# Performance work log

Hardware: AMD Instinct MI355X
Metric: run time of the kernel (lower is better)

## Reference

```python
import jax, jax.numpy as jnp
import numpy as np

N = 50000   # nodes
E = 600000  # edges (avg degree 12)
D = 128     # node feature dim (input == hidden so residual applies)
R = 7       # num_relation
G = 32      # num graphs in the batch
L = 3       # layers
W_SCALE = 0.02


def setup_inputs() -> dict:
    key = jax.random.key(0)
    ks = jax.random.split(key, 5 + 2 * L)
    inp = {
        "x": jax.random.normal(ks[0], (N, D), jnp.float32),
        "node_in": jax.random.randint(ks[1], (E,), 0, N),
        "node_out": jax.random.randint(ks[2], (E,), 0, N),
        "relation": jax.random.randint(ks[3], (E,), 0, R),
        "edge_weight": jnp.ones((E,), jnp.float32),
        "node2graph": jnp.sort(jax.random.randint(ks[4], (N,), 0, G)),
        "num_node": N,
        "num_graphs": G,
    }
    for i in range(L):
        inp[f"sl_w{i}"] = jax.random.normal(ks[5 + 2 * i], (D, D), jnp.float32) * W_SCALE
        inp[f"sl_b{i}"] = jnp.zeros((D,), jnp.float32)
        inp[f"lin_w{i}"] = jax.random.normal(ks[6 + 2 * i], (R * D, D), jnp.float32) * W_SCALE
        inp[f"lin_b{i}"] = jnp.zeros((D,), jnp.float32)
    return inp


def _gearnet(x, edge_weight, params, node_in, node_out, relation, node2graph,
             num_node, num_graphs):
    # relation-keyed scatter index: node_out * R + relation
    idx = node_out * R + relation  # [E]
    h = x
    for (sl_w, sl_b, lin_w, lin_b) in params:
        din = h.shape[1]
        msg = h[node_in] * edge_weight[:, None]                           # [E, din] gather
        agg = jax.ops.segment_sum(msg, idx, num_segments=num_node * R)    # [N*R, din] scatter_add
        upd = agg.reshape(num_node, R * din)                              # [N, R*din]
        out = jax.nn.relu(upd @ lin_w + lin_b + h @ sl_w + sl_b)          # combine: linear + self_loop, relu
        h = out + h                                                        # short_cut residual (shapes match)
    node_feature = h
    graph_feature = jax.ops.segment_sum(node_feature, node2graph, num_segments=num_graphs)  # SumReadout
    return graph_feature, node_feature


def reference(x, node_in, node_out, relation, edge_weight, node2graph,
              sl_w0, sl_b0, lin_w0, lin_b0,
              sl_w1, sl_b1, lin_w1, lin_b1,
              sl_w2, sl_b2, lin_w2, lin_b2,
              num_node, num_graphs):
    params = [(sl_w0, sl_b0, lin_w0, lin_b0),
              (sl_w1, sl_b1, lin_w1, lin_b1),
              (sl_w2, sl_b2, lin_w2, lin_b2)]
    return _gearnet(x, edge_weight, params, node_in, node_out, relation,
                    node2graph, num_node, num_graphs)
```

## Files before the change

### kernel.cpp

```cpp
#include <hip/hip_runtime.h>
#include <hip/hip_bf16.h>

#define NN 50000
#define EE 600000
#define DD 128
#define RR 7
#define SS 8
#define GG 32
#define NSEG (NN * RR)
#define NB1 ((NSEG + 1023) / 1024)

typedef float f32x4 __attribute__((ext_vector_type(4)));
typedef float f32x2 __attribute__((ext_vector_type(2)));
typedef short short8 __attribute__((ext_vector_type(8)));
typedef unsigned short u16x8 __attribute__((ext_vector_type(8)));

static __device__ __forceinline__ unsigned short f2bf(float f) {
    union { float f; unsigned u; } v; v.f = f;
    unsigned r = v.u + 0x7fff + ((v.u >> 16) & 1);
    return (unsigned short)(r >> 16);
}
static __device__ __forceinline__ float bf2f(unsigned short u) {
    union { unsigned u; float f; } v; v.u = ((unsigned)u) << 16;
    return v.f;
}

__global__ void prep_w2(const float* __restrict__ lin_w, const float* __restrict__ sl_w,
                        const float* __restrict__ lin_b, const float* __restrict__ sl_b,
                        unsigned short* __restrict__ Wt2, float* __restrict__ bias) {
    int idx = blockIdx.x * 256 + threadIdx.x;
    if (idx < DD) bias[idx] = lin_b[idx] + sl_b[idx];
    if (idx >= 1024 * DD) return;
    int j = idx >> 7;
    int k = idx & 127;
    int slot = j >> 7, dout = j & 127;
    float w = (slot < 7) ? lin_w[(slot * DD + k) * DD + dout] : sl_w[k * DD + dout];
    Wt2[(size_t)j * DD + k] = f2bf(w);
}

__global__ void zero_misc(int* __restrict__ cc, int* __restrict__ slop, float* __restrict__ gf) {
    int i = blockIdx.x * 256 + threadIdx.x;
    if (i < 2 * NSEG) cc[i] = 0;
    if (i < 16) slop[i] = 0;
    if (i < GG * DD) gf[i] = 0.f;
}

__global__ void hist(const int* __restrict__ node_out, const int* __restrict__ rel,
                     int* __restrict__ counts) {
    int e = blockIdx.x * 256 + threadIdx.x;
    if (e >= EE) return;
    atomicAdd(&counts[node_out[e] * RR + rel[e]], 1);
}

__global__ __launch_bounds__(256) void scan1(const int* __restrict__ counts,
                                             int* __restrict__ start, int* __restrict__ bsum) {
    __shared__ int s[256];
    int tid = threadIdx.x;
    int base = blockIdx.x * 1024 + tid * 4;
    int v[4], sum = 0;
    #pragma unroll
    for (int j = 0; j < 4; ++j) {
        v[j] = (base + j < NSEG) ? counts[base + j] : 0;
        sum += v[j];
    }
    s[tid] = sum; __syncthreads();
    for (int off = 1; off < 256; off <<= 1) {
        int t = (tid >= off) ? s[tid - off] : 0;
        __syncthreads();
        s[tid] += t;
        __syncthreads();
    }
    int run = s[tid] - sum;
    if (tid == 255) bsum[blockIdx.x] = s[255];
    #pragma unroll
    for (int j = 0; j < 4; ++j) {
        if (base + j < NSEG) { start[base + j] = run; run += v[j]; }
    }
}

__global__ __launch_bounds__(512) void scan2(int* __restrict__ bsum) {
    __shared__ int s[512];
    int tid = threadIdx.x;
    int v = (tid < NB1) ? bsum[tid] : 0;
    s[tid] = v; __syncthreads();
    for (int off = 1; off < 512; off <<= 1) {
        int t = (tid >= off) ? s[tid - off] : 0;
        __syncthreads();
        s[tid] += t;
        __syncthreads();
    }
    if (tid < NB1) bsum[tid] = s[tid] - v;
}

__global__ void scan3(const int* __restrict__ start, const int* __restrict__ bsum,
                      const int* __restrict__ counts, int2* __restrict__ segd) {
    int i = blockIdx.x * 256 + threadIdx.x;
    if (i < NSEG) segd[i] = make_int2(start[i] + bsum[i >> 10], counts[i]);
}

__global__ void fill(const int* __restrict__ node_in, const int* __restrict__ node_out,
                     const int* __restrict__ rel, const float* __restrict__ ew,
                     const int2* __restrict__ segd, int* __restrict__ cursor,
                     int2* __restrict__ edges) {
    int e = blockIdx.x * 256 + threadIdx.x;
    if (e >= EE) return;
    int seg = node_out[e] * RR + rel[e];
    int pos = segd[seg].x + atomicAdd(&cursor[seg], 1);
    edges[pos] = make_int2((rel[e] << 16) | node_in[e], __float_as_int(ew[e]));
}

__global__ void init_hb(const float* __restrict__ x, unsigned short* __restrict__ hb) {
    int t = blockIdx.x * 256 + threadIdx.x;
    if (t >= NN * 32) return;
    f32x4 v = ((const f32x4*)x)[t];
    unsigned long long pack = (unsigned long long)f2bf(v.x)
                            | ((unsigned long long)f2bf(v.y) << 16)
                            | ((unsigned long long)f2bf(v.z) << 32)
                            | ((unsigned long long)f2bf(v.w) << 48);
    ((unsigned long long*)hb)[t] = pack;
}

__global__ __launch_bounds__(256) void gemm_p(
        const unsigned short* __restrict__ hb,
        const unsigned short* __restrict__ Wt2,
        unsigned short* __restrict__ P) {
    int tid = threadIdx.x;
    int wid = tid >> 6, lane = tid & 63;
    int wr = wid >> 1, wc = wid & 1;
    int lm = lane & 15, lg = lane >> 4;
    int bm0 = blockIdx.x * 128;

    short8 af[4][4];
    #pragma unroll
    for (int mi = 0; mi < 4; ++mi) {
        int gr = bm0 + wr * 64 + mi * 16 + lm;
        #pragma unroll
        for (int ks = 0; ks < 4; ++ks) {
            short8 t = {};
            if (gr < NN) t = *(const short8*)(hb + (size_t)gr * DD + ks * 32 + lg * 8);
            af[mi][ks] = t;
        }
    }
    for (int cb = 0; cb < 8; ++cb) {
        f32x4 acc[4][4] = {};
        #pragma unroll
        for (int ks = 0; ks < 4; ++ks) {
            short8 bfr[4];
            #pragma unroll
            for (int ni = 0; ni < 4; ++ni)
                bfr[ni] = *(const short8*)(Wt2 + (size_t)(cb * 128 + wc * 64 + ni * 16 + lm) * DD
                                           + ks * 32 + lg * 8);
            #pragma unroll
            for (int mi = 0; mi < 4; ++mi)
                #pragma unroll
                for (int ni = 0; ni < 4; ++ni)
                    acc[mi][ni] = __builtin_amdgcn_mfma_f32_16x16x32_bf16(af[mi][ks], bfr[ni], acc[mi][ni], 0, 0, 0);
        }
        #pragma unroll
        for (int mi = 0; mi < 4; ++mi) {
            #pragma unroll
            for (int v = 0; v < 4; ++v) {
                int gm = bm0 + wr * 64 + mi * 16 + lg * 4 + v;
                if (gm >= NN) continue;
                #pragma unroll
                for (int ni = 0; ni < 4; ++ni) {
                    int j = cb * 128 + wc * 64 + ni * 16 + lm;
                    P[(size_t)gm * 1024 + j] = f2bf(acc[mi][ni][v]);
                }
            }
        }
    }
}

#define PROW(r) (const unsigned*)(P + (size_t)((((r).x & 0xFFFF) << 3) | ((r).x >> 16)) * DD + lane * 2)
__global__ __launch_bounds__(256) void gather_p(
        const unsigned short* __restrict__ P,
        const int2* __restrict__ segd,
        const int2* __restrict__ edges,
        const float* __restrict__ bias,
        const unsigned short* __restrict__ hb_in,
        unsigned short* __restrict__ hb_out,
        float* __restrict__ nf,
        int last) {
    int tid = threadIdx.x;
    int wv = tid >> 6, lane = tid & 63;
    int node = blockIdx.x * 4 + wv;
    int st = segd[node * RR].x;
    int2 s6 = segd[node * RR + 6];
    int end = s6.x + s6.y;

    float ax = 0.f, ay = 0.f;
    int2 r0 = edges[st];
    int2 r1 = edges[st + 1];
    int2 r2 = edges[st + 2];
    int2 r3 = edges[st + 3];
    int2 r4 = edges[st + 4];
    unsigned hv0 = *PROW(r0);
    unsigned hv1 = *PROW(r1);
    unsigned hv2 = *PROW(r2);
    unsigned hv3 = *PROW(r3);
    for (int i = st; i < end; ++i) {
        int2 r5 = edges[i + 5];
        unsigned hv4 = *PROW(r4);
        float w = __int_as_float(r0.y);
        ax += bf2f((unsigned short)(hv0 & 0xFFFF)) * w;
        ay += bf2f((unsigned short)(hv0 >> 16)) * w;
        r0 = r1; r1 = r2; r2 = r3; r3 = r4; r4 = r5;
        hv0 = hv1; hv1 = hv2; hv2 = hv3; hv3 = hv4;
    }
    unsigned hs = *(const unsigned*)(P + ((size_t)node * 8 + 7) * DD + lane * 2);
    float bx = bias[lane * 2], by = bias[lane * 2 + 1];
    unsigned hp = ((const unsigned*)hb_in)[(size_t)node * 64 + lane];
    float hpx = bf2f((unsigned short)(hp & 0xFFFF));
    float hpy = bf2f((unsigned short)(hp >> 16));
    float vx = fmaxf(ax + bf2f((unsigned short)(hs & 0xFFFF)) + bx, 0.f) + hpx;
    float vy = fmaxf(ay + bf2f((unsigned short)(hs >> 16)) + by, 0.f) + hpy;
    if (last)
        ((f32x2*)nf)[(size_t)node * 64 + lane] = (f32x2){vx, vy};
    else
        ((unsigned*)hb_out)[(size_t)node * 64 + lane] =
            (unsigned)f2bf(vx) | ((unsigned)f2bf(vy) << 16);
}

__global__ __launch_bounds__(256) void readout(const float* __restrict__ h,
                                               const int* __restrict__ n2g,
                                               float* __restrict__ gf) {
    int c0 = blockIdx.x * 128;
    int rg = threadIdx.x >> 5, d4 = threadIdx.x & 31;
    f32x4 acc = {0.f, 0.f, 0.f, 0.f};
    int cur = -1;
    #pragma unroll 4
    for (int it = 0; it < 16; ++it) {
        int row = c0 + it * 8 + rg;
        if (row >= NN) break;
        int g = n2g[row];
        if (g != cur) {
            if (cur >= 0) {
                atomicAdd(&gf[cur * DD + d4 * 4 + 0], acc.x);
                atomicAdd(&gf[cur * DD + d4 * 4 + 1], acc.y);
                atomicAdd(&gf[cur * DD + d4 * 4 + 2], acc.z);
                atomicAdd(&gf[cur * DD + d4 * 4 + 3], acc.w);
            }
            cur = g;
            acc = (f32x4){0.f, 0.f, 0.f, 0.f};
        }
        acc += ((const f32x4*)h)[(size_t)row * 32 + d4];
    }
    if (cur >= 0) {
        atomicAdd(&gf[cur * DD + d4 * 4 + 0], acc.x);
        atomicAdd(&gf[cur * DD + d4 * 4 + 1], acc.y);
        atomicAdd(&gf[cur * DD + d4 * 4 + 2], acc.z);
        atomicAdd(&gf[cur * DD + d4 * 4 + 3], acc.w);
    }
}

extern "C" void kernel_launch(void* const* d_in, const int* in_sizes, int n_in,
                              void* d_out, int out_size, void* d_ws, size_t ws_size,
                              hipStream_t stream) {
    const float* x      = (const float*)d_in[0];
    const int* node_in  = (const int*)d_in[1];
    const int* node_out = (const int*)d_in[2];
    const int* relation = (const int*)d_in[3];
    const float* ew     = (const float*)d_in[4];
    const int* n2g      = (const int*)d_in[5];
    const float* sl_w[3]  = {(const float*)d_in[8],  (const float*)d_in[12], (const float*)d_in[16]};
    const float* sl_b[3]  = {(const float*)d_in[9],  (const float*)d_in[13], (const float*)d_in[17]};
    const float* lin_w[3] = {(const float*)d_in[10], (const float*)d_in[14], (const float*)d_in[18]};
    const float* lin_b[3] = {(const float*)d_in[11], (const float*)d_in[15], (const float*)d_in[19]};

    float* out = (float*)d_out;
    float* gf = out;
    float* nf = out + GG * DD;

    char* ws = (char*)d_ws;
    size_t off = 0;
    unsigned short* P  = (unsigned short*)(ws + off); off += (size_t)NN * 1024 * 2;
    unsigned short* hb0 = (unsigned short*)(ws + off); off += (size_t)NN * DD * 2;
    unsigned short* hb1 = (unsigned short*)(ws + off); off += (size_t)NN * DD * 2;
    unsigned short* Wt2 = (unsigned short*)(ws + off); off += (size_t)3 * 1024 * DD * 2;
    float* bias = (float*)(ws + off);            off += 3 * DD * 4;
    int* counts = (int*)(ws + off);              off += (size_t)NSEG * 4;
    int* cursor = (int*)(ws + off);              off += (size_t)NSEG * 4;
    int* start  = (int*)(ws + off);              off += (size_t)NSEG * 4;
    int2* segd  = (int2*)(ws + off);             off += (size_t)NSEG * 8;
    int* bsum   = (int*)(ws + off);              off += 512 * 4;
    int2* edges = (int2*)(ws + off);             off += (size_t)(EE + 8) * 8;

    for (int l = 0; l < 3; ++l)
        prep_w2<<<512, 256, 0, stream>>>(lin_w[l], sl_w[l], lin_b[l], sl_b[l],
                                         Wt2 + (size_t)l * 1024 * DD, bias + l * DD);

    zero_misc<<<(2 * NSEG + 255) / 256, 256, 0, stream>>>(counts, (int*)(edges + EE), gf);
    hist<<<(EE + 255) / 256, 256, 0, stream>>>(node_out, relation, counts);
    scan1<<<NB1, 256, 0, stream>>>(counts, start, bsum);
    scan2<<<1, 512, 0, stream>>>(bsum);
    scan3<<<(NSEG + 255) / 256, 256, 0, stream>>>(start, bsum, counts, segd);
    fill<<<(EE + 255) / 256, 256, 0, stream>>>(node_in, node_out, relation, ew,
                                               segd, cursor, edges);
    init_hb<<<(NN * 32) / 256, 256, 0, stream>>>(x, hb0);

    unsigned short* hbs[2] = { hb0, hb1 };
    for (int l = 0; l < 3; ++l) {
        gemm_p<<<(NN + 127) / 128, 256, 0, stream>>>(
            hbs[l & 1], Wt2 + (size_t)l * 1024 * DD, P);
        gather_p<<<NN / 4, 256, 0, stream>>>(
            P, segd, edges, bias + l * DD, hbs[l & 1], hbs[(l + 1) & 1],
            nf, l == 2 ? 1 : 0);
    }
    readout<<<(NN + 127) / 128, 256, 0, stream>>>(nf, n2g, gf);
}
```

Baseline: 392.7 us.

## Bucket edges per destination node and split gather across half-waves

Edge CSR is now keyed by destination node instead of node*relation, which shrinks the histogram, scan and segment arrays sevenfold. The gather kernel has each half-wave process alternate edges with 8-byte loads of four features per lane, then combines the halves with a cross-lane shuffle. The three weight-prep launches are merged into one. Summation order within a node changes and the half-wave split adds predication for odd edge counts.

After: 364.3 us (median of 2 runs). 1.08x faster.

```diff
diff --git a/kernel.cpp b/kernel.cpp
--- a/kernel.cpp
+++ b/kernel.cpp
@@ -5,15 +5,12 @@
 #define EE 600000
 #define DD 128
 #define RR 7
-#define SS 8
 #define GG 32
-#define NSEG (NN * RR)
-#define NB1 ((NSEG + 1023) / 1024)
+#define NB1 ((NN + 1023) / 1024)
 
 typedef float f32x4 __attribute__((ext_vector_type(4)));
 typedef float f32x2 __attribute__((ext_vector_type(2)));
 typedef short short8 __attribute__((ext_vector_type(8)));
-typedef unsigned short u16x8 __attribute__((ext_vector_type(8)));
 
 static __device__ __forceinline__ unsigned short f2bf(float f) {
     union { float f; unsigned u; } v; v.f = f;
@@ -25,31 +22,39 @@
     return v.f;
 }
 
-__global__ void prep_w2(const float* __restrict__ lin_w, const float* __restrict__ sl_w,
-                        const float* __restrict__ lin_b, const float* __restrict__ sl_b,
+__global__ void prep_w2(const float* lw0, const float* lw1, const float* lw2,
+                        const float* sw0, const float* sw1, const float* sw2,
+                        const float* lb0, const float* lb1, const float* lb2,
+                        const float* sb0, const float* sb1, const float* sb2,
                         unsigned short* __restrict__ Wt2, float* __restrict__ bias) {
-    int idx = blockIdx.x * 256 + threadIdx.x;
-    if (idx < DD) bias[idx] = lin_b[idx] + sl_b[idx];
+    int l = blockIdx.x >> 9;
+    int idx = (blockIdx.x & 511) * 256 + threadIdx.x;
+    const float* lin_w = l == 0 ? lw0 : (l == 1 ? lw1 : lw2);
+    const float* sl_w  = l == 0 ? sw0 : (l == 1 ? sw1 : sw2);
+    if (idx < DD) {
+        const float* lin_b = l == 0 ? lb0 : (l == 1 ? lb1 : lb2);
+        const float* sl_b  = l == 0 ? sb0 : (l == 1 ? sb1 : sb2);
+        bias[l * DD + idx] = lin_b[idx] + sl_b[idx];
+    }
     if (idx >= 1024 * DD) return;
     int j = idx >> 7;
     int k = idx & 127;
     int slot = j >> 7, dout = j & 127;
     float w = (slot < 7) ? lin_w[(slot * DD + k) * DD + dout] : sl_w[k * DD + dout];
-    Wt2[(size_t)j * DD + k] = f2bf(w);
+    Wt2[(size_t)l * 1024 * DD + (size_t)j * DD + k] = f2bf(w);
 }
 
 __global__ void zero_misc(int* __restrict__ cc, int* __restrict__ slop, float* __restrict__ gf) {
     int i = blockIdx.x * 256 + threadIdx.x;
-    if (i < 2 * NSEG) cc[i] = 0;
+    if (i < 2 * NN) cc[i] = 0;
     if (i < 16) slop[i] = 0;
     if (i < GG * DD) gf[i] = 0.f;
 }
 
-__global__ void hist(const int* __restrict__ node_out, const int* __restrict__ rel,
-                     int* __restrict__ counts) {
+__global__ void hist(const int* __restrict__ node_out, int* __restrict__ counts) {
     int e = blockIdx.x * 256 + threadIdx.x;
     if (e >= EE) return;
-    atomicAdd(&counts[node_out[e] * RR + rel[e]], 1);
+    atomicAdd(&counts[node_out[e]], 1);
 }
 
 __global__ __launch_bounds__(256) void scan1(const int* __restrict__ counts,
@@ -60,7 +65,7 @@
     int v[4], sum = 0;
     #pragma unroll
     for (int j = 0; j < 4; ++j) {
-        v[j] = (base + j < NSEG) ? counts[base + j] : 0;
+        v[j] = (base + j < NN) ? counts[base + j] : 0;
         sum += v[j];
     }
     s[tid] = sum; __syncthreads();
@@ -74,16 +79,16 @@
     if (tid == 255) bsum[blockIdx.x] = s[255];
     #pragma unroll
     for (int j = 0; j < 4; ++j) {
-        if (base + j < NSEG) { start[base + j] = run; run += v[j]; }
-    }
-}
-
-__global__ __launch_bounds__(512) void scan2(int* __restrict__ bsum) {
-    __shared__ int s[512];
+        if (base + j < NN) { start[base + j] = run; run += v[j]; }
+    }
+}
+
+__global__ __launch_bounds__(64) void scan2(int* __restrict__ bsum) {
+    __shared__ int s[64];
     int tid = threadIdx.x;
     int v = (tid < NB1) ? bsum[tid] : 0;
     s[tid] = v; __syncthreads();
-    for (int off = 1; off < 512; off <<= 1) {
+    for (int off = 1; off < 64; off <<= 1) {
         int t = (tid >= off) ? s[tid - off] : 0;
         __syncthreads();
         s[tid] += t;
@@ -95,7 +100,7 @@
 __global__ void scan3(const int* __restrict__ start, const int* __restrict__ bsum,
                       const int* __restrict__ counts, int2* __restrict__ segd) {
     int i = blockIdx.x * 256 + threadIdx.x;
-    if (i < NSEG) segd[i] = make_int2(start[i] + bsum[i >> 10], counts[i]);
+    if (i < NN) segd[i] = make_int2(start[i] + bsum[i >> 10], counts[i]);
 }
 
 __global__ void fill(const int* __restrict__ node_in, const int* __restrict__ node_out,
@@ -104,7 +109,7 @@
                      int2* __restrict__ edges) {
     int e = blockIdx.x * 256 + threadIdx.x;
     if (e >= EE) return;
-    int seg = node_out[e] * RR + rel[e];
+    int seg = node_out[e];
     int pos = segd[seg].x + atomicAdd(&cursor[seg], 1);
     edges[pos] = make_int2((rel[e] << 16) | node_in[e], __float_as_int(ew[e]));
 }
@@ -172,7 +177,7 @@
     }
 }
 
-#define PROW(r) (const unsigned*)(P + (size_t)((((r).x & 0xFFFF) << 3) | ((r).x >> 16)) * DD + lane * 2)
+#define PR(r) ((const uint2*)(P + (size_t)(((((r).x & 0xFFFF) << 3) | ((r).x >> 16))) * DD) + l5)
 __global__ __launch_bounds__(256) void gather_p(
         const unsigned short* __restrict__ P,
         const int2* __restrict__ segd,
@@ -184,42 +189,54 @@
         int last) {
     int tid = threadIdx.x;
     int wv = tid >> 6, lane = tid & 63;
+    int h = lane >> 5, l5 = lane & 31;
     int node = blockIdx.x * 4 + wv;
-    int st = segd[node * RR].x;
-    int2 s6 = segd[node * RR + 6];
-    int end = s6.x + s6.y;
-
-    float ax = 0.f, ay = 0.f;
-    int2 r0 = edges[st];
-    int2 r1 = edges[st + 1];
-    int2 r2 = edges[st + 2];
-    int2 r3 = edges[st + 3];
-    int2 r4 = edges[st + 4];
-    unsigned hv0 = *PROW(r0);
-    unsigned hv1 = *PROW(r1);
-    unsigned hv2 = *PROW(r2);
-    unsigned hv3 = *PROW(r3);
-    for (int i = st; i < end; ++i) {
-        int2 r5 = edges[i + 5];
-        unsigned hv4 = *PROW(r4);
-        float w = __int_as_float(r0.y);
-        ax += bf2f((unsigned short)(hv0 & 0xFFFF)) * w;
-        ay += bf2f((unsigned short)(hv0 >> 16)) * w;
-        r0 = r1; r1 = r2; r2 = r3; r3 = r4; r4 = r5;
-        hv0 = hv1; hv1 = hv2; hv2 = hv3; hv3 = hv4;
-    }
-    unsigned hs = *(const unsigned*)(P + ((size_t)node * 8 + 7) * DD + lane * 2);
-    float bx = bias[lane * 2], by = bias[lane * 2 + 1];
-    unsigned hp = ((const unsigned*)hb_in)[(size_t)node * 64 + lane];
-    float hpx = bf2f((unsigned short)(hp & 0xFFFF));
-    float hpy = bf2f((unsigned short)(hp >> 16));
-    float vx = fmaxf(ax + bf2f((unsigned short)(hs & 0xFFFF)) + bx, 0.f) + hpx;
-    float vy = fmaxf(ay + bf2f((unsigned short)(hs >> 16)) + by, 0.f) + hpy;
-    if (last)
-        ((f32x2*)nf)[(size_t)node * 64 + lane] = (f32x2){vx, vy};
-    else
-        ((unsigned*)hb_out)[(size_t)node * 64 + lane] =
-            (unsigned)f2bf(vx) | ((unsigned)f2bf(vy) << 16);
+    int2 sd = segd[node];
+    int st = sd.x, cnt = sd.y;
+    int base = st + h;
+    int mmax = (cnt + 1) >> 1;
+
+    f32x4 ac = {0.f, 0.f, 0.f, 0.f};
+    int2 r0 = edges[base];
+    int2 r1 = edges[base + 2];
+    int2 r2 = edges[base + 4];
+    uint2 hv0 = *PR(r0);
+    uint2 hv1 = *PR(r1);
+    for (int i = 0; i < mmax; ++i) {
+        int2 r3 = edges[base + 2 * i + 6];
+        uint2 hv2 = *PR(r2);
+        if (h + 2 * i < cnt) {
+            float w = __int_as_float(r0.y);
+            ac.x += bf2f((unsigned short)(hv0.x & 0xFFFF)) * w;
+            ac.y += bf2f((unsigned short)(hv0.x >> 16)) * w;
+            ac.z += bf2f((unsigned short)(hv0.y & 0xFFFF)) * w;
+            ac.w += bf2f((unsigned short)(hv0.y >> 16)) * w;
+        }
+        r0 = r1; r1 = r2; r2 = r3;
+        hv0 = hv1; hv1 = hv2;
+    }
+    ac.x += __shfl_xor(ac.x, 32);
+    ac.y += __shfl_xor(ac.y, 32);
+    ac.z += __shfl_xor(ac.z, 32);
+    ac.w += __shfl_xor(ac.w, 32);
+
+    if (h == 0) {
+        uint2 hs = *((const uint2*)(P + ((size_t)node * 8 + 7) * DD) + l5);
+        f32x4 b4 = ((const f32x4*)bias)[l5];
+        uint2 hp = ((const uint2*)hb_in)[(size_t)node * 32 + l5];
+        float o0 = fmaxf(ac.x + bf2f((unsigned short)(hs.x & 0xFFFF)) + b4.x, 0.f) + bf2f((unsigned short)(hp.x & 0xFFFF));
+        float o1 = fmaxf(ac.y + bf2f((unsigned short)(hs.x >> 16))   + b4.y, 0.f) + bf2f((unsigned short)(hp.x >> 16));
+        float o2 = fmaxf(ac.z + bf2f((unsigned short)(hs.y & 0xFFFF)) + b4.z, 0.f) + bf2f((unsigned short)(hp.y & 0xFFFF));
+        float o3 = fmaxf(ac.w + bf2f((unsigned short)(hs.y >> 16))   + b4.w, 0.f) + bf2f((unsigned short)(hp.y >> 16));
+        if (last) {
+            ((f32x4*)nf)[(size_t)node * 32 + l5] = (f32x4){o0, o1, o2, o3};
+        } else {
+            uint2 pk;
+            pk.x = (unsigned)f2bf(o0) | ((unsigned)f2bf(o1) << 16);
+            pk.y = (unsigned)f2bf(o2) | ((unsigned)f2bf(o3) << 16);
+            ((uint2*)hb_out)[(size_t)node * 32 + l5] = pk;
+        }
+    }
 }
 
 __global__ __launch_bounds__(256) void readout(const float* __restrict__ h,
@@ -263,10 +280,6 @@
     const int* relation = (const int*)d_in[3];
     const float* ew     = (const float*)d_in[4];
     const int* n2g      = (const int*)d_in[5];
-    const float* sl_w[3]  = {(const float*)d_in[8],  (const float*)d_in[12], (const float*)d_in[16]};
-    const float* sl_b[3]  = {(const float*)d_in[9],  (const float*)d_in[13], (const float*)d_in[17]};
-    const float* lin_w[3] = {(const float*)d_in[10], (const float*)d_in[14], (const float*)d_in[18]};
-    const float* lin_b[3] = {(const float*)d_in[11], (const float*)d_in[15], (const float*)d_in[19]};
 
     float* out = (float*)d_out;
     float* gf = out;
@@ -279,22 +292,25 @@
     unsigned short* hb1 = (unsigned short*)(ws + off); off += (size_t)NN * DD * 2;
     unsigned short* Wt2 = (unsigned short*)(ws + off); off += (size_t)3 * 1024 * DD * 2;
     float* bias = (float*)(ws + off);            off += 3 * DD * 4;
-    int* counts = (int*)(ws + off);              off += (size_t)NSEG * 4;
-    int* cursor = (int*)(ws + off);              off += (size_t)NSEG * 4;
-    int* start  = (int*)(ws + off);              off += (size_t)NSEG * 4;
-    int2* segd  = (int2*)(ws + off);             off += (size_t)NSEG * 8;
-    int* bsum   = (int*)(ws + off);              off += 512 * 4;
+    int* counts = (int*)(ws + off);              off += (size_t)NN * 4;
+    int* cursor = (int*)(ws + off);              off += (size_t)NN * 4;
+    int* start  = (int*)(ws + off);              off += (size_t)NN * 4;
+    int2* segd  = (int2*)(ws + off);             off += (size_t)NN * 8;
+    int* bsum   = (int*)(ws + off);              off += 64 * 4;
     int2* edges = (int2*)(ws + off);             off += (size_t)(EE + 8) * 8;
 
-    for (int l = 0; l < 3; ++l)
-        prep_w2<<<512, 256, 0, stream>>>(lin_w[l], sl_w[l], lin_b[l], sl_b[l],
-                                         Wt2 + (size_t)l * 1024 * DD, bias + l * DD);
-
-    zero_misc<<<(2 * NSEG + 255) / 256, 256, 0, stream>>>(counts, (int*)(edges + EE), gf);
-    hist<<<(EE + 255) / 256, 256, 0, stream>>>(node_out, relation, counts);
+    prep_w2<<<3 * 512, 256, 0, stream>>>(
+        (const float*)d_in[10], (const float*)d_in[14], (const float*)d_in[18],
+        (const float*)d_in[8],  (const float*)d_in[12], (const float*)d_in[16],
+        (const float*)d_in[11], (const float*)d_in[15], (const float*)d_in[19],
+        (const float*)d_in[9],  (const float*)d_in[13], (const float*)d_in[17],
+        Wt2, bias);
+
+    zero_misc<<<(2 * NN + 255) / 256, 256, 0, stream>>>(counts, (int*)(edges + EE), gf);
+    hist<<<(EE + 255) / 256, 256, 0, stream>>>(node_out, counts);
     scan1<<<NB1, 256, 0, stream>>>(counts, start, bsum);
-    scan2<<<1, 512, 0, stream>>>(bsum);
-    scan3<<<(NSEG + 255) / 256, 256, 0, stream>>>(start, bsum, counts, segd);
+    scan2<<<1, 64, 0, stream>>>(bsum);
+    scan3<<<(NN + 255) / 256, 256, 0, stream>>>(start, bsum, counts, segd);
     fill<<<(EE + 255) / 256, 256, 0, stream>>>(node_in, node_out, relation, ew,
                                                segd, cursor, edges);
     init_hb<<<(NN * 32) / 256, 256, 0, stream>>>(x, hb0);
```
